# Kernel tuning notes

Hardware: AMD Instinct MI355X
Metric: run time of the kernel (lower is better)

The kernel has to match this reference:

```python
import jax, jax.numpy as jnp
import numpy as np

HID = 256
HEADS = 8
DPH = HID // HEADS  # 32
N = 65536
E = 262144


def _ln(x, g, b):
    m = jnp.mean(x, axis=-1, keepdims=True)
    v = jnp.var(x, axis=-1, keepdims=True)
    return (x - m) * jax.lax.rsqrt(v + 1e-5) * g + b


def _gelu(x):
    return jax.nn.gelu(x, approximate=False)


def _mlp2(x, W1, b1, W2, b2, act):
    return act(x @ W1 + b1) @ W2 + b2


def setup_inputs() -> dict:
    key = jax.random.key(0)
    ks = jax.random.split(key, 32)
    d = {}
    d["x"] = jax.random.normal(ks[0], (N, HID), jnp.float32)
    d["edge_index"] = jax.random.randint(ks[1], (2, E), 0, N, dtype=jnp.int32)
    d["edge_attr"] = jax.random.normal(ks[2], (E, 7), jnp.float32)
    i = 3
    def p(shape, s=0.02):
        nonlocal i
        out = jax.random.normal(ks[i], shape, jnp.float32) * s
        i += 1
        return out
    for nm, (din, dh, do) in [("q", (2 * HID + 3, 2 * HID, HID)),
                              ("k", (2 * HID + 3, 2 * HID, HID)),
                              ("v", (2 * HID + 3, 2 * HID, HID)),
                              ("s", (4, 64, HEADS)),
                              ("f", (HID, 2 * HID, HID))]:
        d[nm + "W1"] = p((din, dh))
        d[nm + "b1"] = jnp.zeros((dh,), jnp.float32)
        d[nm + "W2"] = p((dh, do))
        d[nm + "b2"] = jnp.zeros((do,), jnp.float32)
    d["ln_g"] = jnp.ones((HID,), jnp.float32)
    d["ln_b"] = jnp.zeros((HID,), jnp.float32)
    d["rW"] = p((2 * HID, HID))
    d["rb"] = jnp.zeros((HID,), jnp.float32)
    return d


def reference(x, edge_index, edge_attr,
              qW1, qb1, qW2, qb2,
              kW1, kb1, kW2, kb2,
              vW1, vb1, vW2, vb2,
              sW1, sb1, sW2, sb2,
              ln_g, ln_b, rW, rb,
              fW1, fb1, fW2, fb2):
    n_nodes = x.shape[0]
    original_x = x
    residual = x
    xn = _ln(x, ln_g, ln_b)

    src = edge_index[0]
    dst = edge_index[1]
    # gather endpoint features, concat with molecular edge feats -> [E, 2*HID+3]
    comb = jnp.concatenate([xn[src], xn[dst], edge_attr[:, :3]], axis=1)

    Q = _mlp2(comb, qW1, qb1, qW2, qb2, _gelu).reshape(-1, HEADS, DPH)
    K = _mlp2(comb, kW1, kb1, kW2, kb2, _gelu).reshape(-1, HEADS, DPH)
    V = _mlp2(comb, vW1, vb1, vW2, vb2, _gelu).reshape(-1, HEADS, DPH)

    scale = jnp.sqrt(jnp.float32(DPH))
    scores = jnp.einsum('ehd,egd->ehg', Q, K) / scale  # [E, H, H]
    bias = _mlp2(edge_attr[:, 3:7], sW1, sb1, sW2, sb2, jax.nn.relu)[:, :, None]  # [E, H, 1]
    attn = jax.nn.softmax(scores + bias, axis=1)  # softmax over dim=1, as in torch code
    wv = jnp.einsum('ehg,egd->ehd', attn, V).reshape(-1, HID)  # [E, HID]

    # scatter-mean to target nodes (edge_index[1])
    sums = jax.ops.segment_sum(wv, dst, num_segments=n_nodes)
    cnt = jax.ops.segment_sum(jnp.ones((wv.shape[0],), wv.dtype), dst, num_segments=n_nodes)
    out = sums / jnp.maximum(cnt, 1.0)[:, None]

    x1 = residual + out
    fused = jnp.concatenate([x1, original_x], axis=-1)
    x2 = x1 + (fused @ rW + rb)
    x3 = x2 + _mlp2(_ln(x2, ln_g, ln_b), fW1, fb1, fW2, fb2, _gelu)
    return x3
```

## Files before the change

kernel.cpp:

```cpp
#include <hip/hip_runtime.h>

#define N_NODES 65536
#define N_EDGES 262144

typedef unsigned short u16;
typedef unsigned char u8;
typedef float f32x4 __attribute__((ext_vector_type(4)));
typedef _Float16 h2 __attribute__((ext_vector_type(2)));
typedef _Float16 v8h __attribute__((ext_vector_type(8)));

__device__ __forceinline__ u16 f2h(float f) {
  return __builtin_bit_cast(u16, (_Float16)f);
}
__device__ __forceinline__ u8 f2e5m2(float f) {
  _Float16 h = (_Float16)f;
  u16 hb = __builtin_bit_cast(u16, h);
  hb = (u16)(hb + 0x7F + ((hb >> 8) & 1));
  return (u8)(hb >> 8);
}
__device__ __forceinline__ void dec4(unsigned d, float* o) {
  o[0] = (float)__builtin_bit_cast(_Float16, (u16)((d << 8) & 0xFF00u));
  o[1] = (float)__builtin_bit_cast(_Float16, (u16)(d & 0xFF00u));
  o[2] = (float)__builtin_bit_cast(_Float16, (u16)((d >> 8) & 0xFF00u));
  o[3] = (float)__builtin_bit_cast(_Float16, (u16)((d >> 16) & 0xFF00u));
}
__device__ __forceinline__ h2 e5lo(unsigned d) {
  return __builtin_bit_cast(h2, __builtin_amdgcn_perm(d, 0u, 0x05000400u));
}
__device__ __forceinline__ h2 e5hi(unsigned d) {
  return __builtin_bit_cast(h2, __builtin_amdgcn_perm(d, 0u, 0x07000600u));
}
__device__ __forceinline__ float gelu_s(float x) {
  float e = __expf(1.702f * x);
  return x - __fdividef(x, e + 1.0f);
}
__device__ __forceinline__ float gelu_f(float x) {
  float y = 1.5957691216057308f * (x + 0.044715f * x * x * x);
  float e = __expf(y);
  return x - __fdividef(x, e + 1.0f);
}
__device__ __forceinline__ void gld16(const u16* g, u16* l) {
  __builtin_amdgcn_global_load_lds(
      (const __attribute__((address_space(1))) void*)g,
      (__attribute__((address_space(3))) void*)l, 16, 0, 0);
}

__global__ __launch_bounds__(256) void ln_kernel(const float* __restrict__ x,
                                                 const float* __restrict__ g,
                                                 const float* __restrict__ b,
                                                 u16* __restrict__ out) {
  int row = blockIdx.x * 4 + (threadIdx.x >> 6);
  int lane = threadIdx.x & 63;
  float4 v = ((const float4*)(x + (size_t)row * 256))[lane];
  float s = v.x + v.y + v.z + v.w;
  float s2 = v.x * v.x + v.y * v.y + v.z * v.z + v.w * v.w;
#pragma unroll
  for (int off = 1; off < 64; off <<= 1) {
    s += __shfl_xor(s, off, 64);
    s2 += __shfl_xor(s2, off, 64);
  }
  float mean = s * (1.0f / 256.0f);
  float var = s2 * (1.0f / 256.0f) - mean * mean;
  float rs = rsqrtf(var + 1e-5f);
  float4 gv = ((const float4*)g)[lane];
  float4 bv = ((const float4*)b)[lane];
  ushort4 o;
  o.x = f2h((v.x - mean) * rs * gv.x + bv.x);
  o.y = f2h((v.y - mean) * rs * gv.y + bv.y);
  o.z = f2h((v.z - mean) * rs * gv.z + bv.z);
  o.w = f2h((v.w - mean) * rs * gv.w + bv.w);
  *(ushort4*)(out + (size_t)row * 256 + lane * 4) = o;
}

template <typename Epi>
__global__ __launch_bounds__(256) void gemm_bt(const u16* __restrict__ A,
                                               const u16* __restrict__ BT,
                                               int K, Epi epi) {
  __shared__ __align__(16) u16 sA[128 * 48];
  __shared__ __align__(16) u16 sB[128 * 48];
  const int tm = blockIdx.x * 128, tn = blockIdx.y * 128;
  const int t = threadIdx.x;
  const int wave = t >> 6, lane = t & 63;
  const int lrow = lane & 15, quad = lane >> 4;
  const int wrow = (wave & 1) * 64, wcol = (wave >> 1) * 64;
  const int r = t >> 2, c = (t & 3) << 3;
  f32x4 acc[4][4];
  const f32x4 z = {0.f, 0.f, 0.f, 0.f};
#pragma unroll
  for (int i = 0; i < 4; ++i)
#pragma unroll
    for (int j = 0; j < 4; ++j) acc[i][j] = z;
  for (int k0 = 0; k0 < K; k0 += 32) {
    *(uint4*)&sA[r * 48 + c] = *(const uint4*)&A[(size_t)(tm + r) * K + k0 + c];
    *(uint4*)&sA[(r + 64) * 48 + c] = *(const uint4*)&A[(size_t)(tm + r + 64) * K + k0 + c];
    *(uint4*)&sB[r * 48 + c] = *(const uint4*)&BT[(size_t)(tn + r) * K + k0 + c];
    *(uint4*)&sB[(r + 64) * 48 + c] = *(const uint4*)&BT[(size_t)(tn + r + 64) * K + k0 + c];
    __syncthreads();
    v8h af[4], bfv[4];
#pragma unroll
    for (int i = 0; i < 4; ++i) af[i] = *(const v8h*)&sA[(wrow + i * 16 + lrow) * 48 + quad * 8];
#pragma unroll
    for (int j = 0; j < 4; ++j) bfv[j] = *(const v8h*)&sB[(wcol + j * 16 + lrow) * 48 + quad * 8];
#pragma unroll
    for (int i = 0; i < 4; ++i)
#pragma unroll
      for (int j = 0; j < 4; ++j)
        acc[i][j] = __builtin_amdgcn_mfma_f32_16x16x32_f16(af[i], bfv[j], acc[i][j], 0, 0, 0);
    __syncthreads();
  }
#pragma unroll
  for (int i = 0; i < 4; ++i)
#pragma unroll
    for (int j = 0; j < 4; ++j)
#pragma unroll
      for (int rg = 0; rg < 4; ++rg)
        epi(tm + wrow + i * 16 + quad * 4 + rg, tn + wcol + j * 16 + lrow, acc[i][j][rg]);
}

#define GEMM_DBUF(K_)                                                                    \
  const int t = threadIdx.x;                                                             \
  const int wave = t >> 6, lane = t & 63;                                                \
  const int lrow = lane & 15, quad = lane >> 4;                                          \
  const int wrow = (wave & 1) * 64, wcol = (wave >> 1) * 64;                             \
  const int sa0 = 2 * wave, sa1 = 2 * wave + 1;                                          \
  const u16* pa0 = A + (size_t)(tm + sa0 * 16 + lrow) * (K_) + quad * 8;                 \
  const u16* pa1 = A + (size_t)(tm + sa1 * 16 + lrow) * (K_) + quad * 8;                 \
  const u16* pb0 = BT + (size_t)(tn + sa0 * 16 + lrow) * (K_) + quad * 8;                \
  const u16* pb1 = BT + (size_t)(tn + sa1 * 16 + lrow) * (K_) + quad * 8;                \
  f32x4 acc[4][4];                                                                       \
  {                                                                                      \
    const f32x4 z = {0.f, 0.f, 0.f, 0.f};                                                \
    _Pragma("unroll") for (int i = 0; i < 4; ++i)                                        \
        _Pragma("unroll") for (int j = 0; j < 4; ++j) acc[i][j] = z;                     \
  }                                                                                      \
  gld16(pa0, &sAB[sa0 * 512]);                                                           \
  gld16(pa1, &sAB[sa1 * 512]);                                                           \
  gld16(pb0, &sAB[4096 + sa0 * 512]);                                                    \
  gld16(pb1, &sAB[4096 + sa1 * 512]);                                                    \
  pa0 += 32; pa1 += 32; pb0 += 32; pb1 += 32;                                            \
  __syncthreads();                                                                       \
  int cur = 0;                                                                           \
  _Pragma("unroll") for (int k0 = 32; k0 < (K_); k0 += 32) {                             \
    const int nxt = cur ^ 1;                                                             \
    gld16(pa0, &sAB[nxt * 8192 + sa0 * 512]);                                            \
    gld16(pa1, &sAB[nxt * 8192 + sa1 * 512]);                                            \
    gld16(pb0, &sAB[nxt * 8192 + 4096 + sa0 * 512]);                                     \
    gld16(pb1, &sAB[nxt * 8192 + 4096 + sa1 * 512]);                                     \
    pa0 += 32; pa1 += 32; pb0 += 32; pb1 += 32;                                          \
    v8h af[4], bfv[4];                                                                   \
    _Pragma("unroll") for (int i = 0; i < 4; ++i) af[i] =                                \
        *(const v8h*)&sAB[cur * 8192 + ((wave & 1) * 4 + i) * 512 + lane * 8];           \
    _Pragma("unroll") for (int j = 0; j < 4; ++j) bfv[j] =                               \
        *(const v8h*)&sAB[cur * 8192 + 4096 + ((wave >> 1) * 4 + j) * 512 + lane * 8];   \
    _Pragma("unroll") for (int i = 0; i < 4; ++i)                                        \
        _Pragma("unroll") for (int j = 0; j < 4; ++j) acc[i][j] =                        \
            __builtin_amdgcn_mfma_f32_16x16x32_f16(af[i], bfv[j], acc[i][j], 0, 0, 0);   \
    __syncthreads();                                                                     \
    cur = nxt;                                                                           \
  }                                                                                      \
  {                                                                                      \
    v8h af[4], bfv[4];                                                                   \
    _Pragma("unroll") for (int i = 0; i < 4; ++i) af[i] =                                \
        *(const v8h*)&sAB[cur * 8192 + ((wave & 1) * 4 + i) * 512 + lane * 8];           \
    _Pragma("unroll") for (int j = 0; j < 4; ++j) bfv[j] =                               \
        *(const v8h*)&sAB[cur * 8192 + 4096 + ((wave >> 1) * 4 + j) * 512 + lane * 8];   \
    _Pragma("unroll") for (int i = 0; i < 4; ++i)                                        \
        _Pragma("unroll") for (int j = 0; j < 4; ++j) acc[i][j] =                        \
            __builtin_amdgcn_mfma_f32_16x16x32_f16(af[i], bfv[j], acc[i][j], 0, 0, 0);   \
  }

__global__ __launch_bounds__(256) void gemm2_ab(const u16* __restrict__ A,
                                                const u16* __restrict__ BT,
                                                const float* __restrict__ b1cat,
                                                u8* __restrict__ out) {
  __shared__ __align__(16) u16 sAB[16384];
  const int bid = blockIdx.x;
  const int local = bid >> 3;
  const int mt = (bid & 7) * 64 + local / 24;
  const int nt = local % 24;
  const int tm = mt * 128, tn = nt * 128;
  GEMM_DBUF(256)
  __syncthreads();
  float bj[4];
#pragma unroll
  for (int j = 0; j < 4; ++j)
    bj[j] = (nt < 12) ? b1cat[tn + wcol + j * 16 + lrow] : 0.f;
  u8* sb = (u8*)sAB;
#pragma unroll
  for (int i = 0; i < 4; ++i)
#pragma unroll
    for (int j = 0; j < 4; ++j)
#pragma unroll
      for (int rg = 0; rg < 4; ++rg)
        sb[(wrow + i * 16 + quad * 4 + rg) * 136 + wcol + j * 16 + lrow] =
            f2e5m2(acc[i][j][rg] + bj[j]);
  __syncthreads();
  {
    int ir = t >> 1, sg = t & 1;
    const u8* srcp = &sb[ir * 136 + sg * 64];
    uint2* dstp = (uint2*)(out + (size_t)(tm + ir) * 3072 + tn + sg * 64);
#pragma unroll
    for (int q = 0; q < 8; ++q) dstp[q] = *(const uint2*)(srcp + q * 8);
  }
}

struct EpiX2 {
  float* x2;
  const float* x1;
  const float* rb;
  __device__ void operator()(int m, int n, float v) const {
    x2[(size_t)m * 256 + n] = v + rb[n] + x1[(size_t)m * 256 + n];
  }
};
struct EpiHf {
  u16* hf;
  const float* b1;
  __device__ void operator()(int m, int n, float v) const {
    hf[(size_t)m * 512 + n] = f2h(gelu_f(v + b1[n]));
  }
};
struct EpiOut {
  float* out;
  const float* b2;
  const float* x2;
  __device__ void operator()(int m, int n, float v) const {
    out[(size_t)m * 256 + n] = v + b2[n] + x2[(size_t)m * 256 + n];
  }
};

__global__ void prep_w1catT(u16* __restrict__ out, const float* __restrict__ qW1,
                            const float* __restrict__ kW1, const float* __restrict__ vW1) {
  int cIdx = blockIdx.x;
  int rIdx = threadIdx.x;
  int sec = cIdx >> 9;
  int h = cIdx & 511;
  int mlp = sec % 3;
  const float* W1 = (mlp == 0) ? qW1 : (mlp == 1) ? kW1 : vW1;
  int rowoff = (sec < 3) ? 0 : 256;
  out[(size_t)cIdx * 256 + rIdx] = f2h(W1[(size_t)(rowoff + rIdx) * 512 + h]);
}
__global__ void prep_w2T(u16* __restrict__ out, const float* __restrict__ qW2,
                         const float* __restrict__ kW2, const float* __restrict__ vW2) {
  int row = blockIdx.x;
  int m = row >> 8, n = row & 255;
  const float* W2 = (m == 0) ? qW2 : (m == 1) ? kW2 : vW2;
  for (int k = threadIdx.x; k < 512; k += 256)
    out[(size_t)row * 512 + k] = f2h(W2[(size_t)k * 256 + n]);
}
__global__ void transpose_cast(u16* __restrict__ out, const float* __restrict__ in, int K, int Nn) {
  int n = blockIdx.x;
  for (int k = threadIdx.x; k < K; k += blockDim.x)
    out[(size_t)n * K + k] = f2h(in[(size_t)k * Nn + n]);
}
__global__ void prep_w1e16(u16* __restrict__ out, const float* __restrict__ qW1,
                           const float* __restrict__ kW1, const float* __restrict__ vW1) {
  int b = blockIdx.x;
  int m = b / 3, r = b % 3;
  const float* W1 = (m == 0) ? qW1 : (m == 1) ? kW1 : vW1;
  out[(size_t)b * 512 + threadIdx.x] = f2h(W1[(size_t)(512 + r) * 512 + threadIdx.x]);
}
__global__ void prep_b1cat(float* __restrict__ out, const float* __restrict__ qb1,
                           const float* __restrict__ kb1, const float* __restrict__ vb1) {
  int idx = blockIdx.x * 256 + threadIdx.x;
  const float* b = (idx < 512) ? qb1 : (idx < 1024) ? kb1 : vb1;
  out[idx] = b[idx & 511];
}

__global__ __launch_bounds__(256) void bias_kernel(const float* __restrict__ eattr,
                                                   const float* __restrict__ sW1,
                                                   const float* __restrict__ sb1,
                                                   const float* __restrict__ sW2,
                                                   const float* __restrict__ sb2,
                                                   float* __restrict__ biasb) {
  int e = blockIdx.x * 256 + threadIdx.x;
  const float* ea = eattr + (size_t)e * 7;
  float a0 = ea[3], a1 = ea[4], a2 = ea[5], a3 = ea[6];
  float acc[8];
#pragma unroll
  for (int h = 0; h < 8; ++h) acc[h] = sb2[h];
#pragma unroll 4
  for (int j = 0; j < 64; ++j) {
    float zz = fmaxf(a0 * sW1[j] + a1 * sW1[64 + j] + a2 * sW1[128 + j] + a3 * sW1[192 + j] + sb1[j], 0.f);
#pragma unroll
    for (int h = 0; h < 8; ++h) acc[h] += zz * sW2[j * 8 + h];
  }
  float4* bp = (float4*)(biasb + (size_t)e * 8);
  float4 v0 = {acc[0], acc[1], acc[2], acc[3]};
  float4 v1 = {acc[4], acc[5], acc[6], acc[7]};
  bp[0] = v0;
  bp[1] = v1;
}

__global__ __launch_bounds__(256) void hist_kernel(const int* __restrict__ dst,
                                                   unsigned* __restrict__ cnt) {
  int e = blockIdx.x * 256 + threadIdx.x;
  atomicAdd(&cnt[dst[e]], 1u);
}
__global__ __launch_bounds__(1024) void scan_kernel(const unsigned* __restrict__ cnt,
                                                    unsigned* __restrict__ off,
                                                    unsigned* __restrict__ woff) {
  __shared__ unsigned s_part[1024];
  int t = threadIdx.x;
  unsigned local[64];
  unsigned run = 0;
  const uint4* cp = (const uint4*)(cnt + t * 64);
#pragma unroll
  for (int j = 0; j < 16; ++j) {
    uint4 v = cp[j];
    local[j * 4 + 0] = v.x; local[j * 4 + 1] = v.y;
    local[j * 4 + 2] = v.z; local[j * 4 + 3] = v.w;
  }
#pragma unroll
  for (int j = 0; j < 64; ++j) { unsigned c = local[j]; local[j] = run; run += c; }
  s_part[t] = run;
  __syncthreads();
  for (int d = 1; d < 1024; d <<= 1) {
    unsigned v = (t >= d) ? s_part[t - d] : 0u;
    __syncthreads();
    s_part[t] += v;
    __syncthreads();
  }
  unsigned base = (t == 0) ? 0u : s_part[t - 1];
  for (int j = 0; j < 64; ++j) {
    unsigned o = base + local[j];
    off[t * 64 + j] = o;
    woff[t * 64 + j] = o;
  }
}
__global__ __launch_bounds__(256) void scatter_ids(const int* __restrict__ dst,
                                                   unsigned* __restrict__ woff,
                                                   unsigned* __restrict__ eid) {
  int e = blockIdx.x * 256 + threadIdx.x;
  unsigned pos = atomicAdd(&woff[dst[e]], 1u);
  eid[pos] = (unsigned)e;
}

__global__ __launch_bounds__(256) void qkv_attn(
    const int* __restrict__ eidx, const float* __restrict__ eattr,
    const u8* __restrict__ AB, const u16* __restrict__ W2T, const u16* __restrict__ w1e16,
    const float* __restrict__ qb2, const float* __restrict__ kb2, const float* __restrict__ vb2,
    const float* __restrict__ biasb, u8* __restrict__ wv) {
  __shared__ __align__(16) u8 sQ[64][784];
  __shared__ __align__(16) u8 sRaw[17408];
  __shared__ int s_src[64], s_dst[64];
  __shared__ __align__(16) float s_ea[64][4];
  u16(*sH)[136] = (u16(*)[136])sRaw;
  float(*sS)[8][8] = (float(*)[8][8])sRaw;
  const int t = threadIdx.x;
  const int e0 = blockIdx.x * 64;
  if (t < 64) {
    s_src[t] = eidx[e0 + t];
    s_dst[t] = eidx[N_EDGES + e0 + t];
  } else if (t >= 128 && t < 192) {
    int i = t - 128;
    const float* ea = eattr + (size_t)(e0 + i) * 7;
    s_ea[i][0] = ea[0]; s_ea[i][1] = ea[1]; s_ea[i][2] = ea[2];
  }
  __syncthreads();
  const int i = t & 63, seg = t >> 6;
  const int lane = t & 63, wave = t >> 6;
  const int lrow = lane & 15, quad = lane >> 4;
  const int wrow = (wave & 1) * 32, wcol = (wave >> 1) * 128;
  h2 ea0h, ea1h, ea2h;
  ea0h[0] = ea0h[1] = (_Float16)s_ea[i][0];
  ea1h[0] = ea1h[1] = (_Float16)s_ea[i][1];
  ea2h[0] = ea2h[1] = (_Float16)s_ea[i][2];
  const u8* ABs = AB + (size_t)s_src[i] * 3072 + seg * 32;
  const u8* ABd = AB + (size_t)s_dst[i] * 3072 + 1536 + seg * 32;
#pragma unroll 1
  for (int m = 0; m < 3; ++m) {
    const unsigned* w32 = (const unsigned*)(w1e16 + (size_t)m * 1536);
    const u8* rsB = ABs + m * 512;
    const u8* rdB = ABd + m * 512;
    const u16* Wm = W2T + (size_t)(m * 256 + wcol) * 512;
    f32x4 acc[2][8];
    {
      const f32x4 z = {0.f, 0.f, 0.f, 0.f};
#pragma unroll
      for (int i2 = 0; i2 < 2; ++i2)
#pragma unroll
        for (int j = 0; j < 8; ++j) acc[i2][j] = z;
    }
    for (int k0 = 0; k0 < 512; k0 += 128) {
      {
        alignas(16) unsigned sd[8], dd[8];
        *(uint4*)&sd[0] = *(const uint4*)(rsB + k0);
        *(uint4*)&sd[4] = *(const uint4*)(rsB + k0 + 16);
        *(uint4*)&dd[0] = *(const uint4*)(rdB + k0);
        *(uint4*)&dd[4] = *(const uint4*)(rdB + k0 + 16);
        const int cp0 = (k0 + seg * 32) >> 1;
        alignas(16) unsigned hout[16];
#pragma unroll
        for (int d = 0; d < 8; ++d) {
          int cp = cp0 + d * 2;
          h2 slo = e5lo(sd[d]) + e5lo(dd[d]);
          h2 shi = e5hi(sd[d]) + e5hi(dd[d]);
          slo += ea0h * __builtin_bit_cast(h2, w32[cp]);
          shi += ea0h * __builtin_bit_cast(h2, w32[cp + 1]);
          slo += ea1h * __builtin_bit_cast(h2, w32[256 + cp]);
          shi += ea1h * __builtin_bit_cast(h2, w32[256 + cp + 1]);
          slo += ea2h * __builtin_bit_cast(h2, w32[512 + cp]);
          shi += ea2h * __builtin_bit_cast(h2, w32[512 + cp + 1]);
          float g0 = gelu_s((float)slo[0]), g1 = gelu_s((float)slo[1]);
          float g2 = gelu_s((float)shi[0]), g3 = gelu_s((float)shi[1]);
          hout[d * 2] = (unsigned)f2h(g0) | ((unsigned)f2h(g1) << 16);
          hout[d * 2 + 1] = (unsigned)f2h(g2) | ((unsigned)f2h(g3) << 16);
        }
        uint4* hp = (uint4*)&sH[i][seg * 32];
        hp[0] = *(const uint4*)&hout[0];
        hp[1] = *(const uint4*)&hout[4];
        hp[2] = *(const uint4*)&hout[8];
        hp[3] = *(const uint4*)&hout[12];
      }
      __syncthreads();
#pragma unroll
      for (int ks = 0; ks < 4; ++ks) {
        int kk = ks * 32;
        v8h a0 = *(const v8h*)&sH[wrow + lrow][kk + quad * 8];
        v8h a1 = *(const v8h*)&sH[wrow + 16 + lrow][kk + quad * 8];
#pragma unroll
        for (int j = 0; j < 8; ++j) {
          v8h b = *(const v8h*)&Wm[(size_t)(j * 16 + lrow) * 512 + k0 + kk + quad * 8];
          acc[0][j] = __builtin_amdgcn_mfma_f32_16x16x32_f16(a0, b, acc[0][j], 0, 0, 0);
          acc[1][j] = __builtin_amdgcn_mfma_f32_16x16x32_f16(a1, b, acc[1][j], 0, 0, 0);
        }
      }
      __syncthreads();
    }
    const float* b2 = (m == 0) ? qb2 : (m == 1) ? kb2 : vb2;
#pragma unroll
    for (int i2 = 0; i2 < 2; ++i2)
#pragma unroll
      for (int j = 0; j < 8; ++j)
#pragma unroll
        for (int rg = 0; rg < 4; ++rg) {
          int row = wrow + i2 * 16 + quad * 4 + rg;
          int col = wcol + j * 16 + lrow;
          sQ[row][m * 256 + col] = f2e5m2(acc[i2][j][rg] + b2[col]);
        }
  }
  __syncthreads();
  const int hh = t & 7, ib = t >> 3;
#pragma unroll
  for (int half = 0; half < 2; ++half) {
    const int ii = ib + half * 32;
    alignas(16) unsigned qd[8];
    *(uint4*)&qd[0] = *(const uint4*)&sQ[ii][hh * 32];
    *(uint4*)&qd[4] = *(const uint4*)&sQ[ii][hh * 32 + 16];
    h2 qh[16];
#pragma unroll
    for (int d = 0; d < 8; ++d) { qh[d * 2] = e5lo(qd[d]); qh[d * 2 + 1] = e5hi(qd[d]); }
    float bias = biasb[(size_t)(e0 + ii) * 8 + hh];
    float sc[8];
#pragma unroll
    for (int g = 0; g < 8; ++g) {
      alignas(16) unsigned kd[8];
      *(uint4*)&kd[0] = *(const uint4*)&sQ[ii][256 + g * 32];
      *(uint4*)&kd[4] = *(const uint4*)&sQ[ii][256 + g * 32 + 16];
      h2 acc;
      acc[0] = acc[1] = (_Float16)0.f;
#pragma unroll
      for (int d = 0; d < 8; ++d) {
        acc += qh[d * 2] * e5lo(kd[d]);
        acc += qh[d * 2 + 1] * e5hi(kd[d]);
      }
      sc[g] = (float)acc[0] + (float)acc[1];
    }
#pragma unroll
    for (int g = 0; g < 8; ++g) sS[ii][hh][g] = sc[g] * 0.17677669529663687f + bias;
  }
  __syncthreads();
#pragma unroll
  for (int half = 0; half < 2; ++half) {
    const int ii = ib + half * 32;
    const int g = hh;
    float mx = -1e30f;
#pragma unroll
    for (int h2i = 0; h2i < 8; ++h2i) mx = fmaxf(mx, sS[ii][h2i][g]);
    float ev[8], ssum = 0.f;
#pragma unroll
    for (int h2i = 0; h2i < 8; ++h2i) {
      ev[h2i] = __expf(sS[ii][h2i][g] - mx);
      ssum += ev[h2i];
    }
    float inv = 1.0f / ssum;
#pragma unroll
    for (int h2i = 0; h2i < 8; ++h2i) sS[ii][h2i][g] = ev[h2i] * inv;
  }
  __syncthreads();
#pragma unroll
  for (int half = 0; half < 2; ++half) {
    const int ii = ib + half * 32;
    h2 va[16];
#pragma unroll
    for (int u = 0; u < 16; ++u) va[u][0] = va[u][1] = (_Float16)0.f;
#pragma unroll
    for (int g = 0; g < 8; ++g) {
      float at = sS[ii][hh][g];
      h2 at2;
      at2[0] = at2[1] = (_Float16)at;
      alignas(16) unsigned vd[8];
      *(uint4*)&vd[0] = *(const uint4*)&sQ[ii][512 + g * 32];
      *(uint4*)&vd[4] = *(const uint4*)&sQ[ii][512 + g * 32 + 16];
#pragma unroll
      for (int d = 0; d < 8; ++d) {
        va[d * 2] += at2 * e5lo(vd[d]);
        va[d * 2 + 1] += at2 * e5hi(vd[d]);
      }
    }
    alignas(16) unsigned od[8];
#pragma unroll
    for (int p = 0; p < 8; ++p) {
      unsigned a = __builtin_bit_cast(unsigned, va[p * 2]) + 0x00800080u;
      unsigned b = __builtin_bit_cast(unsigned, va[p * 2 + 1]) + 0x00800080u;
      od[p] = __builtin_amdgcn_perm(b, a, 0x07050301u);
    }
    u8* dp = wv + (size_t)(e0 + ii) * 256 + hh * 32;
    *(uint4*)dp = *(const uint4*)&od[0];
    *(uint4*)(dp + 16) = *(const uint4*)&od[4];
  }
}

__global__ __launch_bounds__(256) void node_gather(const unsigned* __restrict__ off,
                                                   const unsigned* __restrict__ cnt,
                                                   const unsigned* __restrict__ eid,
                                                   const u8* __restrict__ wv,
                                                   const float* __restrict__ x,
                                                   float* __restrict__ x1,
                                                   u16* __restrict__ X1cat) {
  int n = blockIdx.x * 4 + (threadIdx.x >> 6);
  int lane = threadIdx.x & 63;
  unsigned st = off[n], c = cnt[n];
  float a0 = 0.f, a1 = 0.f, a2 = 0.f, a3 = 0.f;
  for (unsigned j = 0; j < c; ++j) {
    unsigned e = eid[st + j];
    unsigned d = *(const unsigned*)(wv + (size_t)e * 256 + lane * 4);
    float f[4];
    dec4(d, f);
    a0 += f[0]; a1 += f[1]; a2 += f[2]; a3 += f[3];
  }
  float inv = 1.0f / fmaxf((float)c, 1.0f);
  float4 xv = *(const float4*)(x + (size_t)n * 256 + lane * 4);
  float4 x1v = {xv.x + a0 * inv, xv.y + a1 * inv, xv.z + a2 * inv, xv.w + a3 * inv};
  *(float4*)(x1 + (size_t)n * 256 + lane * 4) = x1v;
  ushort4 a, bq;
  a.x = f2h(x1v.x); a.y = f2h(x1v.y); a.z = f2h(x1v.z); a.w = f2h(x1v.w);
  bq.x = f2h(xv.x); bq.y = f2h(xv.y); bq.z = f2h(xv.z); bq.w = f2h(xv.w);
  *(ushort4*)(X1cat + (size_t)n * 512 + lane * 4) = a;
  *(ushort4*)(X1cat + (size_t)n * 512 + 256 + lane * 4) = bq;
}

extern "C" void kernel_launch(void* const* d_in, const int* in_sizes, int n_in,
                              void* d_out, int out_size, void* d_ws, size_t ws_size,
                              hipStream_t stream) {
  const float* x = (const float*)d_in[0];
  const int* eidx = (const int*)d_in[1];
  const float* eattr = (const float*)d_in[2];
  const float* qW1 = (const float*)d_in[3];
  const float* qb1 = (const float*)d_in[4];
  const float* qW2 = (const float*)d_in[5];
  const float* qb2 = (const float*)d_in[6];
  const float* kW1 = (const float*)d_in[7];
  const float* kb1 = (const float*)d_in[8];
  const float* kW2 = (const float*)d_in[9];
  const float* kb2 = (const float*)d_in[10];
  const float* vW1 = (const float*)d_in[11];
  const float* vb1 = (const float*)d_in[12];
  const float* vW2 = (const float*)d_in[13];
  const float* vb2 = (const float*)d_in[14];
  const float* sW1 = (const float*)d_in[15];
  const float* sb1 = (const float*)d_in[16];
  const float* sW2 = (const float*)d_in[17];
  const float* sb2 = (const float*)d_in[18];
  const float* fW1 = (const float*)d_in[19];
  const float* fb1 = (const float*)d_in[20];
  const float* fW2 = (const float*)d_in[21];
  const float* fb2 = (const float*)d_in[22];
  const float* lng = (const float*)d_in[23];
  const float* lnb = (const float*)d_in[24];
  const float* rW = (const float*)d_in[25];
  const float* rb = (const float*)d_in[26];

  const size_t N = N_NODES;
  char* ws = (char*)d_ws;
  size_t off_b = 0;
  auto alloc = [&](size_t bytes) {
    void* p = ws + off_b;
    off_b = (off_b + bytes + 255) & ~(size_t)255;
    return p;
  };
  u16* W1catT = (u16*)alloc((size_t)3072 * 256 * 2);
  u16* W2T = (u16*)alloc((size_t)768 * 512 * 2);
  u16* rWT = (u16*)alloc((size_t)256 * 512 * 2);
  u16* fW1T = (u16*)alloc((size_t)512 * 256 * 2);
  u16* fW2T = (u16*)alloc((size_t)256 * 512 * 2);
  u16* w1e16 = (u16*)alloc((size_t)9 * 512 * 2);
  float* b1cat = (float*)alloc((size_t)1536 * 4);
  unsigned* cnt = (unsigned*)alloc(N * 4);
  unsigned* offs = (unsigned*)alloc(N * 4);
  unsigned* woff = (unsigned*)alloc(N * 4);
  unsigned* eid = (unsigned*)alloc((size_t)N_EDGES * 4);
  float* biasb = (float*)alloc((size_t)N_EDGES * 8 * 4);
  u8* AB = (u8*)alloc(N * 3072);
  u16* xn = (u16*)d_out;
  u8* wv = (u8*)d_out;
  float* x1 = (float*)AB;
  u16* X1cat = (u16*)(AB + (size_t)67108864);
  float* x2 = (float*)(AB + (size_t)134217728);
  u16* xn2 = (u16*)AB;
  u16* Hf = (u16*)(AB + (size_t)33554432);

  hipMemsetAsync(cnt, 0, N * 4, stream);
  hist_kernel<<<N_EDGES / 256, 256, 0, stream>>>(eidx + N_EDGES, cnt);
  scan_kernel<<<1, 1024, 0, stream>>>(cnt, offs, woff);
  scatter_ids<<<N_EDGES / 256, 256, 0, stream>>>(eidx + N_EDGES, woff, eid);
  prep_w1catT<<<3072, 256, 0, stream>>>(W1catT, qW1, kW1, vW1);
  prep_w2T<<<768, 256, 0, stream>>>(W2T, qW2, kW2, vW2);
  prep_w1e16<<<9, 512, 0, stream>>>(w1e16, qW1, kW1, vW1);
  prep_b1cat<<<6, 256, 0, stream>>>(b1cat, qb1, kb1, vb1);
  transpose_cast<<<256, 256, 0, stream>>>(rWT, rW, 512, 256);
  transpose_cast<<<512, 256, 0, stream>>>(fW1T, fW1, 256, 512);
  transpose_cast<<<256, 256, 0, stream>>>(fW2T, fW2, 512, 256);
  bias_kernel<<<N_EDGES / 256, 256, 0, stream>>>(eattr, sW1, sb1, sW2, sb2, biasb);

  ln_kernel<<<N_NODES / 4, 256, 0, stream>>>(x, lng, lnb, xn);
  gemm2_ab<<<12288, 256, 0, stream>>>(xn, W1catT, b1cat, AB);
  qkv_attn<<<N_EDGES / 64, 256, 0, stream>>>(eidx, eattr, AB, W2T, w1e16,
                                             qb2, kb2, vb2, biasb, wv);
  node_gather<<<N_NODES / 4, 256, 0, stream>>>(offs, cnt, eid, wv, x, x1, X1cat);
  gemm_bt<<<dim3(N_NODES / 128, 2), 256, 0, stream>>>(X1cat, rWT, 512, EpiX2{x2, x1, rb});
  ln_kernel<<<N_NODES / 4, 256, 0, stream>>>(x2, lng, lnb, xn2);
  gemm_bt<<<dim3(N_NODES / 128, 4), 256, 0, stream>>>(xn2, fW1T, 256, EpiHf{Hf, fb1});
  gemm_bt<<<dim3(N_NODES / 128, 2), 256, 0, stream>>>(Hf, fW2T, 512, EpiOut{(float*)d_out, fb2, x2});
}
```

Measured before the change: 1.947 ms.

## Process edges in destination-sorted order and prefetch next AB chunk in registers

qkv_attn now walks edges in the CSR order given by eid, loading src/dst/edge attributes and bias through the permutation, and writes wv in sorted position. node_gather then reads contiguous wv rows without the eid indirection. The QKV loops are fully unrolled and the next 128-wide AB gather chunk is software-prefetched into registers so its latency overlaps the current chunk's compute. The risks are higher register pressure from unrolling plus prefetch buffers, and a more scattered gather of edge metadata in qkv_attn.

```diff
diff --git a/kernel.cpp b/kernel.cpp
--- a/kernel.cpp
+++ b/kernel.cpp
@@ -337,24 +337,26 @@
 
 __global__ __launch_bounds__(256) void qkv_attn(
     const int* __restrict__ eidx, const float* __restrict__ eattr,
+    const unsigned* __restrict__ eid,
     const u8* __restrict__ AB, const u16* __restrict__ W2T, const u16* __restrict__ w1e16,
     const float* __restrict__ qb2, const float* __restrict__ kb2, const float* __restrict__ vb2,
     const float* __restrict__ biasb, u8* __restrict__ wv) {
   __shared__ __align__(16) u8 sQ[64][784];
   __shared__ __align__(16) u8 sRaw[17408];
   __shared__ int s_src[64], s_dst[64];
+  __shared__ unsigned s_eid[64];
   __shared__ __align__(16) float s_ea[64][4];
   u16(*sH)[136] = (u16(*)[136])sRaw;
   float(*sS)[8][8] = (float(*)[8][8])sRaw;
   const int t = threadIdx.x;
   const int e0 = blockIdx.x * 64;
   if (t < 64) {
-    s_src[t] = eidx[e0 + t];
-    s_dst[t] = eidx[N_EDGES + e0 + t];
-  } else if (t >= 128 && t < 192) {
-    int i = t - 128;
-    const float* ea = eattr + (size_t)(e0 + i) * 7;
-    s_ea[i][0] = ea[0]; s_ea[i][1] = ea[1]; s_ea[i][2] = ea[2];
+    unsigned e = eid[e0 + t];
+    s_eid[t] = e;
+    s_src[t] = eidx[e];
+    s_dst[t] = eidx[N_EDGES + e];
+    const float* ea = eattr + (size_t)e * 7;
+    s_ea[t][0] = ea[0]; s_ea[t][1] = ea[1]; s_ea[t][2] = ea[2];
   }
   __syncthreads();
   const int i = t & 63, seg = t >> 6;
@@ -367,11 +369,14 @@
   ea2h[0] = ea2h[1] = (_Float16)s_ea[i][2];
   const u8* ABs = AB + (size_t)s_src[i] * 3072 + seg * 32;
   const u8* ABd = AB + (size_t)s_dst[i] * 3072 + 1536 + seg * 32;
-#pragma unroll 1
+  uint4 cs0, cs1, cd0, cd1, ns0, ns1, nd0, nd1;
+  cs0 = *(const uint4*)(ABs);
+  cs1 = *(const uint4*)(ABs + 16);
+  cd0 = *(const uint4*)(ABd);
+  cd1 = *(const uint4*)(ABd + 16);
+#pragma unroll
   for (int m = 0; m < 3; ++m) {
     const unsigned* w32 = (const unsigned*)(w1e16 + (size_t)m * 1536);
-    const u8* rsB = ABs + m * 512;
-    const u8* rdB = ABd + m * 512;
     const u16* Wm = W2T + (size_t)(m * 256 + wcol) * 512;
     f32x4 acc[2][8];
     {
@@ -381,13 +386,25 @@
 #pragma unroll
         for (int j = 0; j < 8; ++j) acc[i2][j] = z;
     }
-    for (int k0 = 0; k0 < 512; k0 += 128) {
+#pragma unroll
+    for (int q = 0; q < 4; ++q) {
+      const int c = m * 4 + q;
+      const int k0 = q * 128;
+      if (c < 11) {
+        const int cn = c + 1;
+        const u8* ps = ABs + (cn >> 2) * 512 + (cn & 3) * 128;
+        const u8* pd = ABd + (cn >> 2) * 512 + (cn & 3) * 128;
+        ns0 = *(const uint4*)(ps);
+        ns1 = *(const uint4*)(ps + 16);
+        nd0 = *(const uint4*)(pd);
+        nd1 = *(const uint4*)(pd + 16);
+      }
       {
         alignas(16) unsigned sd[8], dd[8];
-        *(uint4*)&sd[0] = *(const uint4*)(rsB + k0);
-        *(uint4*)&sd[4] = *(const uint4*)(rsB + k0 + 16);
-        *(uint4*)&dd[0] = *(const uint4*)(rdB + k0);
-        *(uint4*)&dd[4] = *(const uint4*)(rdB + k0 + 16);
+        *(uint4*)&sd[0] = cs0;
+        *(uint4*)&sd[4] = cs1;
+        *(uint4*)&dd[0] = cd0;
+        *(uint4*)&dd[4] = cd1;
         const int cp0 = (k0 + seg * 32) >> 1;
         alignas(16) unsigned hout[16];
 #pragma unroll
@@ -426,6 +443,7 @@
         }
       }
       __syncthreads();
+      cs0 = ns0; cs1 = ns1; cd0 = nd0; cd1 = nd1;
     }
     const float* b2 = (m == 0) ? qb2 : (m == 1) ? kb2 : vb2;
 #pragma unroll
@@ -450,7 +468,7 @@
     h2 qh[16];
 #pragma unroll
     for (int d = 0; d < 8; ++d) { qh[d * 2] = e5lo(qd[d]); qh[d * 2 + 1] = e5hi(qd[d]); }
-    float bias = biasb[(size_t)(e0 + ii) * 8 + hh];
+    float bias = biasb[(size_t)s_eid[ii] * 8 + hh];
     float sc[8];
 #pragma unroll
     for (int g = 0; g < 8; ++g) {
@@ -523,7 +541,6 @@
 
 __global__ __launch_bounds__(256) void node_gather(const unsigned* __restrict__ off,
                                                    const unsigned* __restrict__ cnt,
-                                                   const unsigned* __restrict__ eid,
                                                    const u8* __restrict__ wv,
                                                    const float* __restrict__ x,
                                                    float* __restrict__ x1,
@@ -533,8 +550,7 @@
   unsigned st = off[n], c = cnt[n];
   float a0 = 0.f, a1 = 0.f, a2 = 0.f, a3 = 0.f;
   for (unsigned j = 0; j < c; ++j) {
-    unsigned e = eid[st + j];
-    unsigned d = *(const unsigned*)(wv + (size_t)e * 256 + lane * 4);
+    unsigned d = *(const unsigned*)(wv + (size_t)(st + j) * 256 + lane * 4);
     float f[4];
     dec4(d, f);
     a0 += f[0]; a1 += f[1]; a2 += f[2]; a3 += f[3];
@@ -625,9 +641,9 @@
 
   ln_kernel<<<N_NODES / 4, 256, 0, stream>>>(x, lng, lnb, xn);
   gemm2_ab<<<12288, 256, 0, stream>>>(xn, W1catT, b1cat, AB);
-  qkv_attn<<<N_EDGES / 64, 256, 0, stream>>>(eidx, eattr, AB, W2T, w1e16,
+  qkv_attn<<<N_EDGES / 64, 256, 0, stream>>>(eidx, eattr, eid, AB, W2T, w1e16,
                                              qb2, kb2, vb2, biasb, wv);
-  node_gather<<<N_NODES / 4, 256, 0, stream>>>(offs, cnt, eid, wv, x, x1, X1cat);
+  node_gather<<<N_NODES / 4, 256, 0, stream>>>(offs, cnt, wv, x, x1, X1cat);
   gemm_bt<<<dim3(N_NODES / 128, 2), 256, 0, stream>>>(X1cat, rWT, 512, EpiX2{x2, x1, rb});
   ln_kernel<<<N_NODES / 4, 256, 0, stream>>>(x2, lng, lnb, xn2);
   gemm_bt<<<dim3(N_NODES / 128, 4), 256, 0, stream>>>(xn2, fW1T, 256, EpiHf{Hf, fb1});
```

New measurement: 2.751 ms. 41.2% more time.

## Process edges in dst-sorted order and halve qkv_attn tile to 32 edges

Applied to the files above, without the earlier changes.

qkv_attn now reads edges through the dst-sorted eid permutation and writes wv in sorted order, so node_gather reads contiguous wv rows instead of indirect gathers through eid. The edge tile shrinks from 64 to 32 per block, halving shared memory and accumulators, with launch bounds requesting higher occupancy. The trade-off is that each B-fragment load of W2T now feeds only one MFMA instead of two, increasing weight traffic per edge, and the sorted order makes the src gathers more random.

```diff
diff --git a/kernel.cpp b/kernel.cpp
--- a/kernel.cpp
+++ b/kernel.cpp
@@ -335,63 +335,61 @@
   eid[pos] = (unsigned)e;
 }
 
-__global__ __launch_bounds__(256) void qkv_attn(
+__global__ __launch_bounds__(256, 4) void qkv_attn(
     const int* __restrict__ eidx, const float* __restrict__ eattr,
+    const unsigned* __restrict__ eid,
     const u8* __restrict__ AB, const u16* __restrict__ W2T, const u16* __restrict__ w1e16,
     const float* __restrict__ qb2, const float* __restrict__ kb2, const float* __restrict__ vb2,
     const float* __restrict__ biasb, u8* __restrict__ wv) {
-  __shared__ __align__(16) u8 sQ[64][784];
-  __shared__ __align__(16) u8 sRaw[17408];
-  __shared__ int s_src[64], s_dst[64];
-  __shared__ __align__(16) float s_ea[64][4];
+  __shared__ __align__(16) u8 sQ[32][784];
+  __shared__ __align__(16) u8 sRaw[8704];
+  __shared__ int s_src[32], s_dst[32];
+  __shared__ unsigned s_eid[32];
+  __shared__ __align__(16) float s_ea[32][4];
   u16(*sH)[136] = (u16(*)[136])sRaw;
   float(*sS)[8][8] = (float(*)[8][8])sRaw;
   const int t = threadIdx.x;
-  const int e0 = blockIdx.x * 64;
-  if (t < 64) {
-    s_src[t] = eidx[e0 + t];
-    s_dst[t] = eidx[N_EDGES + e0 + t];
-  } else if (t >= 128 && t < 192) {
-    int i = t - 128;
-    const float* ea = eattr + (size_t)(e0 + i) * 7;
-    s_ea[i][0] = ea[0]; s_ea[i][1] = ea[1]; s_ea[i][2] = ea[2];
+  const int e0 = blockIdx.x * 32;
+  if (t < 32) {
+    unsigned e = eid[e0 + t];
+    s_eid[t] = e;
+    s_src[t] = eidx[e];
+    s_dst[t] = eidx[N_EDGES + e];
+    const float* ea = eattr + (size_t)e * 7;
+    s_ea[t][0] = ea[0]; s_ea[t][1] = ea[1]; s_ea[t][2] = ea[2];
   }
   __syncthreads();
-  const int i = t & 63, seg = t >> 6;
+  const int i = t & 31, seg = t >> 5;
   const int lane = t & 63, wave = t >> 6;
   const int lrow = lane & 15, quad = lane >> 4;
-  const int wrow = (wave & 1) * 32, wcol = (wave >> 1) * 128;
+  const int wrow = (wave & 1) * 16, wcol = (wave >> 1) * 128;
   h2 ea0h, ea1h, ea2h;
   ea0h[0] = ea0h[1] = (_Float16)s_ea[i][0];
   ea1h[0] = ea1h[1] = (_Float16)s_ea[i][1];
   ea2h[0] = ea2h[1] = (_Float16)s_ea[i][2];
-  const u8* ABs = AB + (size_t)s_src[i] * 3072 + seg * 32;
-  const u8* ABd = AB + (size_t)s_dst[i] * 3072 + 1536 + seg * 32;
+  const u8* ABs = AB + (size_t)s_src[i] * 3072 + seg * 16;
+  const u8* ABd = AB + (size_t)s_dst[i] * 3072 + 1536 + seg * 16;
 #pragma unroll 1
   for (int m = 0; m < 3; ++m) {
     const unsigned* w32 = (const unsigned*)(w1e16 + (size_t)m * 1536);
     const u8* rsB = ABs + m * 512;
     const u8* rdB = ABd + m * 512;
     const u16* Wm = W2T + (size_t)(m * 256 + wcol) * 512;
-    f32x4 acc[2][8];
+    f32x4 acc[8];
     {
       const f32x4 z = {0.f, 0.f, 0.f, 0.f};
 #pragma unroll
-      for (int i2 = 0; i2 < 2; ++i2)
-#pragma unroll
-        for (int j = 0; j < 8; ++j) acc[i2][j] = z;
+      for (int j = 0; j < 8; ++j) acc[j] = z;
     }
     for (int k0 = 0; k0 < 512; k0 += 128) {
       {
-        alignas(16) unsigned sd[8], dd[8];
+        alignas(16) unsigned sd[4], dd[4];
         *(uint4*)&sd[0] = *(const uint4*)(rsB + k0);
-        *(uint4*)&sd[4] = *(const uint4*)(rsB + k0 + 16);
         *(uint4*)&dd[0] = *(const uint4*)(rdB + k0);
-        *(uint4*)&dd[4] = *(const uint4*)(rdB + k0 + 16);
-        const int cp0 = (k0 + seg * 32) >> 1;
-        alignas(16) unsigned hout[16];
-#pragma unroll
-        for (int d = 0; d < 8; ++d) {
+        const int cp0 = (k0 + seg * 16) >> 1;
+        alignas(16) unsigned hout[8];
+#pragma unroll
+        for (int d = 0; d < 4; ++d) {
           int cp = cp0 + d * 2;
           h2 slo = e5lo(sd[d]) + e5lo(dd[d]);
           h2 shi = e5hi(sd[d]) + e5hi(dd[d]);
@@ -406,51 +404,43 @@
           hout[d * 2] = (unsigned)f2h(g0) | ((unsigned)f2h(g1) << 16);
           hout[d * 2 + 1] = (unsigned)f2h(g2) | ((unsigned)f2h(g3) << 16);
         }
-        uint4* hp = (uint4*)&sH[i][seg * 32];
+        uint4* hp = (uint4*)&sH[i][seg * 16];
         hp[0] = *(const uint4*)&hout[0];
         hp[1] = *(const uint4*)&hout[4];
-        hp[2] = *(const uint4*)&hout[8];
-        hp[3] = *(const uint4*)&hout[12];
       }
       __syncthreads();
 #pragma unroll
       for (int ks = 0; ks < 4; ++ks) {
         int kk = ks * 32;
         v8h a0 = *(const v8h*)&sH[wrow + lrow][kk + quad * 8];
-        v8h a1 = *(const v8h*)&sH[wrow + 16 + lrow][kk + quad * 8];
 #pragma unroll
         for (int j = 0; j < 8; ++j) {
           v8h b = *(const v8h*)&Wm[(size_t)(j * 16 + lrow) * 512 + k0 + kk + quad * 8];
-          acc[0][j] = __builtin_amdgcn_mfma_f32_16x16x32_f16(a0, b, acc[0][j], 0, 0, 0);
-          acc[1][j] = __builtin_amdgcn_mfma_f32_16x16x32_f16(a1, b, acc[1][j], 0, 0, 0);
+          acc[j] = __builtin_amdgcn_mfma_f32_16x16x32_f16(a0, b, acc[j], 0, 0, 0);
         }
       }
       __syncthreads();
     }
     const float* b2 = (m == 0) ? qb2 : (m == 1) ? kb2 : vb2;
 #pragma unroll
-    for (int i2 = 0; i2 < 2; ++i2)
-#pragma unroll
-      for (int j = 0; j < 8; ++j)
-#pragma unroll
-        for (int rg = 0; rg < 4; ++rg) {
-          int row = wrow + i2 * 16 + quad * 4 + rg;
-          int col = wcol + j * 16 + lrow;
-          sQ[row][m * 256 + col] = f2e5m2(acc[i2][j][rg] + b2[col]);
-        }
+    for (int j = 0; j < 8; ++j)
+#pragma unroll
+      for (int rg = 0; rg < 4; ++rg) {
+        int row = wrow + quad * 4 + rg;
+        int col = wcol + j * 16 + lrow;
+        sQ[row][m * 256 + col] = f2e5m2(acc[j][rg] + b2[col]);
+      }
   }
   __syncthreads();
-  const int hh = t & 7, ib = t >> 3;
-#pragma unroll
-  for (int half = 0; half < 2; ++half) {
-    const int ii = ib + half * 32;
+  const int hh = t & 7, ii = t >> 3;
+  {
     alignas(16) unsigned qd[8];
     *(uint4*)&qd[0] = *(const uint4*)&sQ[ii][hh * 32];
     *(uint4*)&qd[4] = *(const uint4*)&sQ[ii][hh * 32 + 16];
     h2 qh[16];
 #pragma unroll
     for (int d = 0; d < 8; ++d) { qh[d * 2] = e5lo(qd[d]); qh[d * 2 + 1] = e5hi(qd[d]); }
-    float bias = biasb[(size_t)(e0 + ii) * 8 + hh];
+    float bias = biasb[(size_t)s_eid[ii] * 8 + hh];
     float sc[8];
 #pragma unroll
     for (int g = 0; g < 8; ++g) {
@@ -470,9 +460,7 @@
     for (int g = 0; g < 8; ++g) sS[ii][hh][g] = sc[g] * 0.17677669529663687f + bias;
   }
   __syncthreads();
-#pragma unroll
-  for (int half = 0; half < 2; ++half) {
-    const int ii = ib + half * 32;
+  {
     const int g = hh;
     float mx = -1e30f;
 #pragma unroll
@@ -488,9 +476,7 @@
     for (int h2i = 0; h2i < 8; ++h2i) sS[ii][h2i][g] = ev[h2i] * inv;
   }
   __syncthreads();
-#pragma unroll
-  for (int half = 0; half < 2; ++half) {
-    const int ii = ib + half * 32;
+  {
     h2 va[16];
 #pragma unroll
     for (int u = 0; u < 16; ++u) va[u][0] = va[u][1] = (_Float16)0.f;
@@ -523,7 +509,6 @@
 
 __global__ __launch_bounds__(256) void node_gather(const unsigned* __restrict__ off,
                                                    const unsigned* __restrict__ cnt,
-                                                   const unsigned* __restrict__ eid,
                                                    const u8* __restrict__ wv,
                                                    const float* __restrict__ x,
                                                    float* __restrict__ x1,
@@ -533,8 +518,7 @@
   unsigned st = off[n], c = cnt[n];
   float a0 = 0.f, a1 = 0.f, a2 = 0.f, a3 = 0.f;
   for (unsigned j = 0; j < c; ++j) {
-    unsigned e = eid[st + j];
-    unsigned d = *(const unsigned*)(wv + (size_t)e * 256 + lane * 4);
+    unsigned d = *(const unsigned*)(wv + (size_t)(st + j) * 256 + lane * 4);
     float f[4];
     dec4(d, f);
     a0 += f[0]; a1 += f[1]; a2 += f[2]; a3 += f[3];
@@ -625,9 +609,9 @@
 
   ln_kernel<<<N_NODES / 4, 256, 0, stream>>>(x, lng, lnb, xn);
   gemm2_ab<<<12288, 256, 0, stream>>>(xn, W1catT, b1cat, AB);
-  qkv_attn<<<N_EDGES / 64, 256, 0, stream>>>(eidx, eattr, AB, W2T, w1e16,
+  qkv_attn<<<N_EDGES / 32, 256, 0, stream>>>(eidx, eattr, eid, AB, W2T, w1e16,
                                              qb2, kb2, vb2, biasb, wv);
-  node_gather<<<N_NODES / 4, 256, 0, stream>>>(offs, cnt, eid, wv, x, x1, X1cat);
+  node_gather<<<N_NODES / 4, 256, 0, stream>>>(offs, cnt, wv, x, x1, X1cat);
   gemm_bt<<<dim3(N_NODES / 128, 2), 256, 0, stream>>>(X1cat, rWT, 512, EpiX2{x2, x1, rb});
   ln_kernel<<<N_NODES / 4, 256, 0, stream>>>(x2, lng, lnb, xn2);
   gemm_bt<<<dim3(N_NODES / 128, 4), 256, 0, stream>>>(xn2, fW1T, 256, EpiHf{Hf, fb1});
```

After: 2.305 ms. 1.18x slower.
